# Performance work log

Hardware: AMD Instinct MI355X
Metric: run time of the kernel (lower is better)

Reference implementation:

```python
import jax, jax.numpy as jnp
import numpy as np

B, N = 128, 2048
QUERY_DIM, NODE_DIM, OUT_DIM = 256, 128, 256
LAMBDA_INIT = 0.8
LN_EPS = 1e-5


def setup_inputs() -> dict:
    key = jax.random.key(0)
    ks = jax.random.split(key, 8)
    fp_vec = jax.random.normal(ks[0], (B, QUERY_DIM), dtype=jnp.float32)
    node_mat = jax.random.normal(ks[1], (B, N, NODE_DIM), dtype=jnp.float32)
    mask = jax.random.uniform(ks[2], (B, N)) < 0.75
    s = 1.0 / np.sqrt(QUERY_DIM)
    Wq1 = jax.random.uniform(ks[3], (NODE_DIM, QUERY_DIM), minval=-s, maxval=s, dtype=jnp.float32)
    Wq2 = jax.random.uniform(ks[4], (NODE_DIM, QUERY_DIM), minval=-s, maxval=s, dtype=jnp.float32)
    s2 = 1.0 / np.sqrt(NODE_DIM)
    Wk = jax.random.uniform(ks[5], (NODE_DIM, NODE_DIM), minval=-s2, maxval=s2, dtype=jnp.float32)
    Wv = jax.random.uniform(ks[6], (OUT_DIM, NODE_DIM), minval=-s2, maxval=s2, dtype=jnp.float32)
    lambda_logit = jnp.zeros((1,), dtype=jnp.float32)
    gamma = jnp.ones((OUT_DIM,), dtype=jnp.float32)
    beta = jnp.zeros((OUT_DIM,), dtype=jnp.float32)
    return {"fp_vec": fp_vec, "node_mat": node_mat, "mask": mask,
            "Wq1": Wq1, "Wq2": Wq2, "Wk": Wk, "Wv": Wv,
            "lambda_logit": lambda_logit, "gamma": gamma, "beta": beta}


def reference(fp_vec, node_mat, mask, Wq1, Wq2, Wk, Wv, lambda_logit, gamma, beta):
    node_dim = node_mat.shape[-1]
    inv_scale = 1.0 / jnp.sqrt(jnp.asarray(node_dim, jnp.float32))
    # projections (torch Linear: y = x @ W.T)
    q1 = fp_vec @ Wq1.T            # (B, node_dim)
    q2 = fp_vec @ Wq2.T            # (B, node_dim)
    k = jnp.einsum('bnd,ed->bne', node_mat, Wk)   # (B, N, node_dim)
    v = jnp.einsum('bnd,od->bno', node_mat, Wv)   # (B, N, out_dim)
    # single-query scores over nodes
    s1 = jnp.einsum('bd,bnd->bn', q1, k) * inv_scale
    s2 = jnp.einsum('bd,bnd->bn', q2, k) * inv_scale
    pad = jnp.where(mask, 0.0, -1e9).astype(s1.dtype)  # (B, N)
    A1 = jax.nn.softmax(s1 + pad, axis=-1)
    A2 = jax.nn.softmax(s2 + pad, axis=-1)
    lam = LAMBDA_INIT + jax.nn.sigmoid(lambda_logit) * 0.2  # (1,)
    A_diff = A1 - lam * A2         # dropout inactive (eval)
    z = jnp.einsum('bn,bno->bo', A_diff, v)  # (B, out_dim)
    # LayerNorm
    mu = jnp.mean(z, axis=-1, keepdims=True)
    var = jnp.mean(jnp.square(z - mu), axis=-1, keepdims=True)
    return (z - mu) * jax.lax.rsqrt(var + LN_EPS) * gamma + beta
```

## Files before the change

kernel.cpp:

```cpp
#include <hip/hip_runtime.h>
#include <hip/hip_bf16.h>
#include <math.h>

#define BB 128
#define NN 2048
#define ND 128
#define QD 256
#define OD 256
#define CHUNKS 8
#define ROWS_PER_CHUNK (NN / CHUNKS)
#define PART_STRIDE 260

__global__ __launch_bounds__(128) void proj_kernel(
    const float* __restrict__ fp_vec, const float* __restrict__ Wq1,
    const float* __restrict__ Wq2, const float* __restrict__ Wk,
    float* __restrict__ qk1g, float* __restrict__ qk2g)
{
  __shared__ __align__(16) float fp_s[QD];
  __shared__ float q1_s[ND];
  __shared__ float q2_s[ND];
  const int b = blockIdx.x, t = threadIdx.x;
  fp_s[t]       = fp_vec[b * QD + t];
  fp_s[t + 128] = fp_vec[b * QD + 128 + t];
  __syncthreads();
  float a1 = 0.f, a2 = 0.f;
  const float4* w1p = (const float4*)(Wq1 + t * QD);
  const float4* w2p = (const float4*)(Wq2 + t * QD);
  #pragma unroll 8
  for (int q = 0; q < QD / 4; ++q) {
    float4 wa = w1p[q], wb = w2p[q];
    float4 f = *(const float4*)&fp_s[q * 4];
    a1 += f.x * wa.x + f.y * wa.y + f.z * wa.z + f.w * wa.w;
    a2 += f.x * wb.x + f.y * wb.y + f.z * wb.z + f.w * wb.w;
  }
  q1_s[t] = a1;
  q2_s[t] = a2;
  __syncthreads();
  float k1 = 0.f, k2 = 0.f;
  #pragma unroll 8
  for (int e = 0; e < ND; ++e) {
    float wv = Wk[e * ND + t];
    k1 += q1_s[e] * wv;
    k2 += q2_s[e] * wv;
  }
  const float inv_scale = 0.08838834764831845f;
  qk1g[b * ND + t] = k1 * inv_scale;
  qk2g[b * ND + t] = k2 * inv_scale;
}

__global__ __launch_bounds__(256) void attn_kernel(
    const float* __restrict__ node, const int* __restrict__ mask,
    const float* __restrict__ qk1g, const float* __restrict__ qk2g,
    float* __restrict__ part)
{
  const int bid = blockIdx.x;
  const int b = bid >> 3;
  const int c = bid & (CHUNKS - 1);
  const int t = threadIdx.x;
  const int wave = t >> 6;
  const int lane = t & 63;
  const int half = lane >> 5;
  const int hl = lane & 31;

  const float4 qk1 = *(const float4*)(qk1g + b * ND + hl * 4);
  const float4 qk2 = *(const float4*)(qk2g + b * ND + hl * 4);

  const int row_base = c * ROWS_PER_CHUNK + wave * 64;
  const float* nb = node + (size_t)b * NN * ND;
  const int* mb = mask + b * NN;

  float m1 = -INFINITY, l1 = 0.f;
  float m2 = -INFINITY, l2 = 0.f;
  float4 w1 = make_float4(0.f, 0.f, 0.f, 0.f);
  float4 w2 = make_float4(0.f, 0.f, 0.f, 0.f);

  #pragma unroll 4
  for (int j = 0; j < 32; ++j) {
    const int row = row_base + 2 * j + half;
    const float4 x = *(const float4*)(nb + (size_t)row * ND + hl * 4);
    const int mk = mb[row];

    float d1 = x.x * qk1.x + x.y * qk1.y + x.z * qk1.z + x.w * qk1.w;
    float d2 = x.x * qk2.x + x.y * qk2.y + x.z * qk2.z + x.w * qk2.w;
    #pragma unroll
    for (int off = 1; off < 32; off <<= 1) {
      d1 += __shfl_xor(d1, off, 64);
      d2 += __shfl_xor(d2, off, 64);
    }
    const float pad = mk ? 0.f : -1e9f;
    const float s1 = d1 + pad;
    const float s2 = d2 + pad;

    {
      const float mn = fmaxf(m1, s1);
      const float cc = __expf(m1 - mn);
      const float p  = __expf(s1 - mn);
      l1 = l1 * cc + p;
      w1.x = w1.x * cc + p * x.x;
      w1.y = w1.y * cc + p * x.y;
      w1.z = w1.z * cc + p * x.z;
      w1.w = w1.w * cc + p * x.w;
      m1 = mn;
    }
    {
      const float mn = fmaxf(m2, s2);
      const float cc = __expf(m2 - mn);
      const float p  = __expf(s2 - mn);
      l2 = l2 * cc + p;
      w2.x = w2.x * cc + p * x.x;
      w2.y = w2.y * cc + p * x.y;
      w2.z = w2.z * cc + p * x.z;
      w2.w = w2.w * cc + p * x.w;
      m2 = mn;
    }
  }

  __shared__ float sm1[8], sl1[8], sm2[8], sl2[8];
  __shared__ __align__(16) float sw1[8][ND];
  __shared__ __align__(16) float sw2[8][ND];
  const int hidx = wave * 2 + half;
  if (hl == 0) { sm1[hidx] = m1; sl1[hidx] = l1; sm2[hidx] = m2; sl2[hidx] = l2; }
  *(float4*)&sw1[hidx][hl * 4] = w1;
  *(float4*)&sw2[hidx][hl * 4] = w2;
  __syncthreads();

  float M1 = -INFINITY, M2 = -INFINITY;
  #pragma unroll
  for (int i = 0; i < 8; ++i) { M1 = fmaxf(M1, sm1[i]); M2 = fmaxf(M2, sm2[i]); }
  float e1[8], e2[8];
  float L1 = 0.f, L2 = 0.f;
  #pragma unroll
  for (int i = 0; i < 8; ++i) {
    e1[i] = __expf(sm1[i] - M1); L1 += sl1[i] * e1[i];
    e2[i] = __expf(sm2[i] - M2); L2 += sl2[i] * e2[i];
  }
  float* po = part + (size_t)bid * PART_STRIDE;
  if (t == 0) { po[0] = M1; po[1] = L1; po[2] = M2; po[3] = L2; }
  if (t < ND) {
    float W1 = 0.f, W2 = 0.f;
    #pragma unroll
    for (int i = 0; i < 8; ++i) {
      W1 += sw1[i][t] * e1[i];
      W2 += sw2[i][t] * e2[i];
    }
    po[4 + t]   = W1;
    po[132 + t] = W2;
  }
}

__global__ __launch_bounds__(256) void finish_kernel(
    const float* __restrict__ part, const float* __restrict__ Wv,
    const float* __restrict__ lambda_logit, const float* __restrict__ gamma,
    const float* __restrict__ beta, float* __restrict__ out)
{
  const int b = blockIdx.x, t = threadIdx.x;
  __shared__ float sm1[CHUNKS], sl1[CHUNKS], sm2[CHUNKS], sl2[CHUNKS];
  __shared__ __align__(16) float wd_s[ND];
  __shared__ float red[8];

  if (t < CHUNKS) {
    const float* pc = part + (size_t)(b * CHUNKS + t) * PART_STRIDE;
    sm1[t] = pc[0]; sl1[t] = pc[1]; sm2[t] = pc[2]; sl2[t] = pc[3];
  }
  __syncthreads();

  float M1 = -INFINITY, M2 = -INFINITY;
  #pragma unroll
  for (int i = 0; i < CHUNKS; ++i) { M1 = fmaxf(M1, sm1[i]); M2 = fmaxf(M2, sm2[i]); }
  float e1[CHUNKS], e2[CHUNKS];
  float L1 = 0.f, L2 = 0.f;
  #pragma unroll
  for (int i = 0; i < CHUNKS; ++i) {
    e1[i] = __expf(sm1[i] - M1); L1 += sl1[i] * e1[i];
    e2[i] = __expf(sm2[i] - M2); L2 += sl2[i] * e2[i];
  }
  const float lam = 0.8f + 0.2f / (1.f + __expf(-lambda_logit[0]));

  if (t < ND) {
    float W1 = 0.f, W2 = 0.f;
    #pragma unroll
    for (int i = 0; i < CHUNKS; ++i) {
      const float* pc = part + (size_t)(b * CHUNKS + i) * PART_STRIDE;
      W1 += pc[4 + t] * e1[i];
      W2 += pc[132 + t] * e2[i];
    }
    wd_s[t] = W1 / L1 - lam * (W2 / L2);
  }
  __syncthreads();

  float z = 0.f;
  const float4* wvp = (const float4*)(Wv + t * ND);
  #pragma unroll 8
  for (int d = 0; d < ND / 4; ++d) {
    const float4 w = wvp[d];
    const float4 f = *(const float4*)&wd_s[d * 4];
    z += f.x * w.x + f.y * w.y + f.z * w.z + f.w * w.w;
  }

  const int wave = t >> 6, lane = t & 63;
  float s = z;
  #pragma unroll
  for (int off = 32; off; off >>= 1) s += __shfl_xor(s, off, 64);
  if (lane == 0) red[wave] = s;
  __syncthreads();
  const float mu = (red[0] + red[1] + red[2] + red[3]) * (1.f / OD);
  const float dz = z - mu;
  float vs = dz * dz;
  #pragma unroll
  for (int off = 32; off; off >>= 1) vs += __shfl_xor(vs, off, 64);
  if (lane == 0) red[wave + 4] = vs;
  __syncthreads();
  const float var = (red[4] + red[5] + red[6] + red[7]) * (1.f / OD);
  out[b * OD + t] = dz * rsqrtf(var + 1e-5f) * gamma[t] + beta[t];
}

extern "C" void kernel_launch(void* const* d_in, const int* in_sizes, int n_in,
                              void* d_out, int out_size, void* d_ws, size_t ws_size,
                              hipStream_t stream) {
  const float* fp_vec = (const float*)d_in[0];
  const float* node   = (const float*)d_in[1];
  const int*   mask   = (const int*)d_in[2];
  const float* Wq1    = (const float*)d_in[3];
  const float* Wq2    = (const float*)d_in[4];
  const float* Wk     = (const float*)d_in[5];
  const float* Wv     = (const float*)d_in[6];
  const float* ll     = (const float*)d_in[7];
  const float* gamma  = (const float*)d_in[8];
  const float* beta   = (const float*)d_in[9];
  float* out = (float*)d_out;

  float* qk1g = (float*)d_ws;
  float* qk2g = qk1g + BB * ND;
  float* part = qk2g + BB * ND;

  proj_kernel<<<BB, 128, 0, stream>>>(fp_vec, Wq1, Wq2, Wk, qk1g, qk2g);
  attn_kernel<<<BB * CHUNKS, 256, 0, stream>>>(node, mask, qk1g, qk2g, part);
  finish_kernel<<<BB, 256, 0, stream>>>(part, Wv, ll, gamma, beta, out);
}
```

Baseline: 239.8 us.

## Fuse query projection into attention kernel and use exp2 with prescaled scores

```diff
diff --git a/kernel.cpp b/kernel.cpp
--- a/kernel.cpp
+++ b/kernel.cpp
@@ -11,46 +11,12 @@
 #define ROWS_PER_CHUNK (NN / CHUNKS)
 #define PART_STRIDE 260
 
-__global__ __launch_bounds__(128) void proj_kernel(
+#define EXP2F(x) __builtin_amdgcn_exp2f(x)
+
+__global__ __launch_bounds__(256) void attn_fused_kernel(
+    const float* __restrict__ node, const int* __restrict__ mask,
     const float* __restrict__ fp_vec, const float* __restrict__ Wq1,
     const float* __restrict__ Wq2, const float* __restrict__ Wk,
-    float* __restrict__ qk1g, float* __restrict__ qk2g)
-{
-  __shared__ __align__(16) float fp_s[QD];
-  __shared__ float q1_s[ND];
-  __shared__ float q2_s[ND];
-  const int b = blockIdx.x, t = threadIdx.x;
-  fp_s[t]       = fp_vec[b * QD + t];
-  fp_s[t + 128] = fp_vec[b * QD + 128 + t];
-  __syncthreads();
-  float a1 = 0.f, a2 = 0.f;
-  const float4* w1p = (const float4*)(Wq1 + t * QD);
-  const float4* w2p = (const float4*)(Wq2 + t * QD);
-  #pragma unroll 8
-  for (int q = 0; q < QD / 4; ++q) {
-    float4 wa = w1p[q], wb = w2p[q];
-    float4 f = *(const float4*)&fp_s[q * 4];
-    a1 += f.x * wa.x + f.y * wa.y + f.z * wa.z + f.w * wa.w;
-    a2 += f.x * wb.x + f.y * wb.y + f.z * wb.z + f.w * wb.w;
-  }
-  q1_s[t] = a1;
-  q2_s[t] = a2;
-  __syncthreads();
-  float k1 = 0.f, k2 = 0.f;
-  #pragma unroll 8
-  for (int e = 0; e < ND; ++e) {
-    float wv = Wk[e * ND + t];
-    k1 += q1_s[e] * wv;
-    k2 += q2_s[e] * wv;
-  }
-  const float inv_scale = 0.08838834764831845f;
-  qk1g[b * ND + t] = k1 * inv_scale;
-  qk2g[b * ND + t] = k2 * inv_scale;
-}
-
-__global__ __launch_bounds__(256) void attn_kernel(
-    const float* __restrict__ node, const int* __restrict__ mask,
-    const float* __restrict__ qk1g, const float* __restrict__ qk2g,
     float* __restrict__ part)
 {
   const int bid = blockIdx.x;
@@ -62,8 +28,42 @@
   const int half = lane >> 5;
   const int hl = lane & 31;
 
-  const float4 qk1 = *(const float4*)(qk1g + b * ND + hl * 4);
-  const float4 qk2 = *(const float4*)(qk2g + b * ND + hl * 4);
+  __shared__ __align__(16) float fp_s[QD];
+  __shared__ __align__(16) float q_s[2][ND];
+  __shared__ __align__(16) float qk_s[2][ND];
+  __shared__ float sm1[8], sl1[8], sm2[8], sl2[8];
+  __shared__ __align__(16) float sw1[8][ND];
+  __shared__ __align__(16) float sw2[8][ND];
+
+  fp_s[t] = fp_vec[b * QD + t];
+  __syncthreads();
+  {
+    const int which = t >> 7;
+    const int r = t & 127;
+    const float4* wp = (const float4*)((which ? Wq2 : Wq1) + r * QD);
+    float a = 0.f;
+    #pragma unroll 8
+    for (int q = 0; q < QD / 4; ++q) {
+      const float4 w = wp[q];
+      const float4 f = *(const float4*)&fp_s[q * 4];
+      a += f.x * w.x + f.y * w.y + f.z * w.z + f.w * w.w;
+    }
+    q_s[which][r] = a;
+  }
+  __syncthreads();
+  {
+    const int which = t >> 7;
+    const int d = t & 127;
+    float k = 0.f;
+    #pragma unroll 8
+    for (int e = 0; e < ND; ++e)
+      k += q_s[which][e] * Wk[e * ND + d];
+    qk_s[which][d] = k * (0.08838834764831845f * 1.4426950408889634f);
+  }
+  __syncthreads();
+
+  const float4 qk1 = *(const float4*)&qk_s[0][hl * 4];
+  const float4 qk2 = *(const float4*)&qk_s[1][hl * 4];
 
   const int row_base = c * ROWS_PER_CHUNK + wave * 64;
   const float* nb = node + (size_t)b * NN * ND;
@@ -93,8 +93,8 @@
 
     {
       const float mn = fmaxf(m1, s1);
-      const float cc = __expf(m1 - mn);
-      const float p  = __expf(s1 - mn);
+      const float cc = EXP2F(m1 - mn);
+      const float p  = EXP2F(s1 - mn);
       l1 = l1 * cc + p;
       w1.x = w1.x * cc + p * x.x;
       w1.y = w1.y * cc + p * x.y;
@@ -104,8 +104,8 @@
     }
     {
       const float mn = fmaxf(m2, s2);
-      const float cc = __expf(m2 - mn);
-      const float p  = __expf(s2 - mn);
+      const float cc = EXP2F(m2 - mn);
+      const float p  = EXP2F(s2 - mn);
       l2 = l2 * cc + p;
       w2.x = w2.x * cc + p * x.x;
       w2.y = w2.y * cc + p * x.y;
@@ -115,9 +115,6 @@
     }
   }
 
-  __shared__ float sm1[8], sl1[8], sm2[8], sl2[8];
-  __shared__ __align__(16) float sw1[8][ND];
-  __shared__ __align__(16) float sw2[8][ND];
   const int hidx = wave * 2 + half;
   if (hl == 0) { sm1[hidx] = m1; sl1[hidx] = l1; sm2[hidx] = m2; sl2[hidx] = l2; }
   *(float4*)&sw1[hidx][hl * 4] = w1;
@@ -131,8 +128,8 @@
   float L1 = 0.f, L2 = 0.f;
   #pragma unroll
   for (int i = 0; i < 8; ++i) {
-    e1[i] = __expf(sm1[i] - M1); L1 += sl1[i] * e1[i];
-    e2[i] = __expf(sm2[i] - M2); L2 += sl2[i] * e2[i];
+    e1[i] = EXP2F(sm1[i] - M1); L1 += sl1[i] * e1[i];
+    e2[i] = EXP2F(sm2[i] - M2); L2 += sl2[i] * e2[i];
   }
   float* po = part + (size_t)bid * PART_STRIDE;
   if (t == 0) { po[0] = M1; po[1] = L1; po[2] = M2; po[3] = L2; }
@@ -171,8 +168,8 @@
   float L1 = 0.f, L2 = 0.f;
   #pragma unroll
   for (int i = 0; i < CHUNKS; ++i) {
-    e1[i] = __expf(sm1[i] - M1); L1 += sl1[i] * e1[i];
-    e2[i] = __expf(sm2[i] - M2); L2 += sl2[i] * e2[i];
+    e1[i] = EXP2F(sm1[i] - M1); L1 += sl1[i] * e1[i];
+    e2[i] = EXP2F(sm2[i] - M2); L2 += sl2[i] * e2[i];
   }
   const float lam = 0.8f + 0.2f / (1.f + __expf(-lambda_logit[0]));
 
@@ -229,11 +226,9 @@
   const float* beta   = (const float*)d_in[9];
   float* out = (float*)d_out;
 
-  float* qk1g = (float*)d_ws;
-  float* qk2g = qk1g + BB * ND;
-  float* part = qk2g + BB * ND;
-
-  proj_kernel<<<BB, 128, 0, stream>>>(fp_vec, Wq1, Wq2, Wk, qk1g, qk2g);
-  attn_kernel<<<BB * CHUNKS, 256, 0, stream>>>(node, mask, qk1g, qk2g, part);
+  float* part = (float*)d_ws;
+
+  attn_fused_kernel<<<BB * CHUNKS, 256, 0, stream>>>(node, mask, fp_vec,
+                                                     Wq1, Wq2, Wk, part);
   finish_kernel<<<BB, 256, 0, stream>>>(part, Wv, ll, gamma, beta, out);
 }
```

New measurement: 249.2 us. 3.9% more time.
